# Kernel optimization log

Hardware: AMD Instinct MI355X
Metric: run time of the kernel (lower is better)

The kernel has to match this reference:

```python
import jax, jax.numpy as jnp
import numpy as np

K = 11      # kernel_size
PAD = 5     # (dilation*(K-1)+1 - 1)//2 with dilation=1


def _unfold(x, k, pad):
    # torch nn.Unfold ordering: channel slowest, then (ki, kj) fastest.
    B, C, H, W = x.shape
    xp = jnp.pad(x, ((0, 0), (0, 0), (pad, pad), (pad, pad)))
    # [B, C, k*k, H, W] -- small fixed loop over the 121 kernel offsets
    cols = jnp.stack([xp[:, :, i:i + H, j:j + W]
                      for i in range(k) for j in range(k)], axis=2)
    return cols.reshape(B, C * k * k, H * W)  # [B, 363, L]


def setup_inputs() -> dict:
    key = jax.random.key(0)
    ks = jax.random.split(key, 4)
    x = jax.random.normal(ks[0], (1, 3, 400, 400), dtype=jnp.float32)
    W1 = jax.random.normal(ks[1], (363, 128), dtype=jnp.float32) * 0.05
    b1 = jnp.zeros((128,), dtype=jnp.float32)
    W2 = jax.random.normal(ks[2], (128, 64), dtype=jnp.float32) * 0.08
    b2 = jnp.zeros((64,), dtype=jnp.float32)
    W3 = jax.random.normal(ks[3], (64, 8), dtype=jnp.float32) * 0.1
    b3 = jnp.zeros((8,), dtype=jnp.float32)
    return {"x": x, "W1": W1, "b1": b1, "W2": W2, "b2": b2, "W3": W3, "b3": b3}


def reference(x, W1, b1, W2, b2, W3, b3):
    B, C, H, W = x.shape
    cols = _unfold(x, K, PAD)                 # [B, 363, H*W]
    h = cols.transpose(0, 2, 1)               # [B, L, 363]
    h = jax.nn.leaky_relu(h @ W1 + b1)        # [B, L, 128], slope 0.01 = torch default
    h = jax.nn.leaky_relu(h @ W2 + b2)        # [B, L, 64]
    h = h @ W3 + b3                           # [B, L, 8]
    # Fold(kernel=1) is a reshape; squeeze(0) + permute -> [H, W, E]
    y = h[0].reshape(H, W, -1)
    # F.normalize(p=2, dim=-1, eps=1e-12)
    n = jnp.maximum(jnp.linalg.norm(y, axis=-1, keepdims=True), 1e-12)
    return y / n
```

## Files before the change

### kernel.cpp

```cpp
#include <hip/hip_runtime.h>
#include <hip/hip_bf16.h>
#include <math.h>

typedef _Float16 f16x8 __attribute__((ext_vector_type(8)));
typedef _Float16 f16x4 __attribute__((ext_vector_type(4)));
typedef float    f32x4 __attribute__((ext_vector_type(4)));

#define IMG   400
#define NPIX  160000
#define NKT1  18
#define W1P   (NKT1*8*64*8)
#define W2P   (4*4*64*8)
#define W3P   (2*64*8)
#define H1S   136
#define H2S   72
#define XPH   1938

__device__ __forceinline__ void async_cp16(const _Float16* g, _Float16* l) {
    __builtin_amdgcn_global_load_lds(
        (const __attribute__((address_space(1))) uint32_t*)g,
        (__attribute__((address_space(3))) uint32_t*)l, 16, 0, 0);
}

__global__ void pack_weights(const float* __restrict__ W1,
                             const float* __restrict__ W2,
                             const float* __restrict__ W3,
                             _Float16* __restrict__ ws)
{
    int i = blockIdx.x * blockDim.x + threadIdx.x;
    if (i < 576 * 128) {
        int kp = i >> 7, n = i & 127;
        int kt = kp >> 5, kl = kp & 31, q = kl >> 3, j = kl & 7;
        int pair = kp >> 4, kj = kp & 15;
        int c = pair / 12, ki = pair % 12;
        int mt = n >> 4, n15 = n & 15;
        int lane = q * 16 + n15;
        float v = (ki < 11 && kj < 11) ? W1[(c * 121 + ki * 11 + kj) * 128 + n] : 0.0f;
        ws[((kt * 8 + mt) * 64 + lane) * 8 + j] = (_Float16)v;
    } else if (i < 576 * 128 + 128 * 64) {
        int e = i - 576 * 128;
        int kp = e >> 6, n = e & 63;
        int kt = kp >> 5, kl = kp & 31, q = kl >> 3, j = kl & 7;
        int mt = n >> 4, n15 = n & 15;
        int lane = q * 16 + n15;
        ws[W1P + ((kt * 4 + mt) * 64 + lane) * 8 + j] = (_Float16)W2[kp * 64 + n];
    } else if (i < 576 * 128 + 128 * 64 + 64 * 16) {
        int e = i - 576 * 128 - 128 * 64;
        int kp = e >> 4, n = e & 15;
        int kt = kp >> 5, kl = kp & 31, q = kl >> 3, j = kl & 7;
        int lane = q * 16 + n;
        float v = (n < 8) ? W3[kp * 8 + n] : 0.0f;
        ws[W1P + W2P + (kt * 64 + lane) * 8 + j] = (_Float16)v;
    }
}

__global__ __launch_bounds__(256, 2) void fused_unfold_mlp(
    const float* __restrict__ x,
    const float* __restrict__ b1,
    const float* __restrict__ b2,
    const float* __restrict__ b3,
    const _Float16* __restrict__ wpack,
    float* __restrict__ out)
{
    __shared__ __align__(16) _Float16 xs[2 * XPH];
    __shared__ __align__(16) _Float16 hb[4 * 32 * H1S];
    __shared__ __align__(16) _Float16 w1s[2 * 4096];

    const int tid  = threadIdx.x;
    const int wave = tid >> 6;
    const int lane = tid & 63;
    const int q    = lane >> 4;
    const int n15  = lane & 15;
    const int bx   = blockIdx.x;
    const int by   = blockIdx.y;

    const _Float16* w1p = wpack;
    const _Float16* w2p = wpack + W1P;
    const _Float16* w3p = wpack + W1P + W2P;

    const int kt0 = (bx + by * 25) % NKT1;

    {
        int seg = wave * 2;
        async_cp16(w1p + kt0 * 4096 + seg * 512 + lane * 8, &w1s[seg * 512]);
        async_cp16(w1p + kt0 * 4096 + (seg + 1) * 512 + lane * 8, &w1s[(seg + 1) * 512]);
    }

    for (int w = tid; w < 3 * 19 * 35; w += 256) {
        int col = w % 35;
        int rc  = w / 35;
        int row = rc % 19, c = rc / 19;
        int gy = by * 8 + row - 5;
        int gx = bx * 16 + col - 6;
        float v = 0.0f;
        if ((unsigned)gy < (unsigned)IMG && (unsigned)gx < (unsigned)IMG)
            v = x[c * NPIX + gy * IMG + gx];
        _Float16 hv = (_Float16)v;
        int base = (c * 19 + row) * 34;
        if (col >= 1)  xs[base + col - 1] = hv;
        if (col <= 33) xs[XPH + base + col] = hv;
    }
    __syncthreads();

    _Float16* hw = &hb[wave * 32 * H1S];

    const uint32_t* xsd = (const uint32_t*)xs;
    const int h = q >> 1;
    const int u = n15 + (n15 & 1) + ((q & 1) << 3);
    const int bdw0 = (n15 & 1) * (XPH / 2) + (u >> 1);
    int bdwt[2];
#pragma unroll
    for (int t = 0; t < 2; ++t)
        bdwt[t] = bdw0 + (wave * 2 + t + h) * 17;

    f32x4 acc1[2][8];
#pragma unroll
    for (int t = 0; t < 2; ++t)
#pragma unroll
        for (int mt = 0; mt < 8; ++mt)
            acc1[t][mt] = (f32x4){0.f, 0.f, 0.f, 0.f};

    int kt = kt0;
    for (int kk = 0; kk < NKT1; ++kk) {
        if (kk) __syncthreads();
        const int buf  = kk & 1;
        const int nbuf = buf ^ 1;
        const int ktn  = (kt + 1 == NKT1) ? 0 : kt + 1;
        if (kk < NKT1 - 1) {
            int seg = wave * 2;
            async_cp16(w1p + ktn * 4096 + seg * 512 + lane * 8,
                       &w1s[nbuf * 4096 + seg * 512]);
            async_cp16(w1p + ktn * 4096 + (seg + 1) * 512 + lane * 8,
                       &w1s[nbuf * 4096 + (seg + 1) * 512]);
        }

        const int d6  = (kt >= 12) ? 2 : (kt >= 6 ? 1 : 0);
        const int m6  = kt - d6 * 6;
        const int rim = (d6 * 19 + 2 * m6) * 17;

        f16x8 bf[2];
#pragma unroll
        for (int t = 0; t < 2; ++t) {
            union { uint32_t u[4]; f16x8 f; } cv;
#pragma unroll
            for (int m = 0; m < 4; ++m)
                cv.u[m] = xsd[bdwt[t] + rim + m];
            bf[t] = cv.f;
        }
        const _Float16* wb = &w1s[buf * 4096];
#pragma unroll
        for (int mt = 0; mt < 8; ++mt) {
            f16x8 af = *(const f16x8*)(wb + (mt * 64 + lane) * 8);
            acc1[0][mt] = __builtin_amdgcn_mfma_f32_16x16x32_f16(af, bf[0], acc1[0][mt], 0, 0, 0);
            acc1[1][mt] = __builtin_amdgcn_mfma_f32_16x16x32_f16(af, bf[1], acc1[1][mt], 0, 0, 0);
        }
        kt = ktn;
    }

    f16x8 af2[4][4];
#pragma unroll
    for (int k2 = 0; k2 < 4; ++k2)
#pragma unroll
        for (int mt = 0; mt < 4; ++mt)
            af2[k2][mt] = *(const f16x8*)(w2p + ((k2 * 4 + mt) * 64 + lane) * 8);
    f16x8 af3[2];
#pragma unroll
    for (int k3 = 0; k3 < 2; ++k3)
        af3[k3] = *(const f16x8*)(w3p + (k3 * 64 + lane) * 8);

#pragma unroll
    for (int mt = 0; mt < 8; ++mt) {
        float4 bb = *(const float4*)(b1 + mt * 16 + q * 4);
#pragma unroll
        for (int t = 0; t < 2; ++t) {
            f16x4 hv;
#pragma unroll
            for (int r = 0; r < 4; ++r) {
                float v = acc1[t][mt][r] + ((const float*)&bb)[r];
                v = fmaxf(v, 0.01f * v);
                hv[r] = (_Float16)v;
            }
            *(f16x4*)(hw + (t * 16 + n15) * H1S + mt * 16 + q * 4) = hv;
        }
    }

    f32x4 acc2[2][4];
#pragma unroll
    for (int t = 0; t < 2; ++t)
#pragma unroll
        for (int mt = 0; mt < 4; ++mt)
            acc2[t][mt] = (f32x4){0.f, 0.f, 0.f, 0.f};

#pragma unroll
    for (int k2 = 0; k2 < 4; ++k2) {
        f16x8 bf[2];
#pragma unroll
        for (int t = 0; t < 2; ++t)
            bf[t] = *(const f16x8*)(hw + (t * 16 + n15) * H1S + k2 * 32 + q * 8);
#pragma unroll
        for (int mt = 0; mt < 4; ++mt) {
            acc2[0][mt] = __builtin_amdgcn_mfma_f32_16x16x32_f16(af2[k2][mt], bf[0], acc2[0][mt], 0, 0, 0);
            acc2[1][mt] = __builtin_amdgcn_mfma_f32_16x16x32_f16(af2[k2][mt], bf[1], acc2[1][mt], 0, 0, 0);
        }
    }

#pragma unroll
    for (int mt = 0; mt < 4; ++mt) {
        float4 bb = *(const float4*)(b2 + mt * 16 + q * 4);
#pragma unroll
        for (int t = 0; t < 2; ++t) {
            f16x4 hv;
#pragma unroll
            for (int r = 0; r < 4; ++r) {
                float v = acc2[t][mt][r] + ((const float*)&bb)[r];
                v = fmaxf(v, 0.01f * v);
                hv[r] = (_Float16)v;
            }
            *(f16x4*)(hw + (t * 16 + n15) * H2S + mt * 16 + q * 4) = hv;
        }
    }

    f32x4 acc3[2];
    acc3[0] = (f32x4){0.f, 0.f, 0.f, 0.f};
    acc3[1] = (f32x4){0.f, 0.f, 0.f, 0.f};
#pragma unroll
    for (int k3 = 0; k3 < 2; ++k3) {
#pragma unroll
        for (int t = 0; t < 2; ++t) {
            f16x8 bf = *(const f16x8*)(hw + (t * 16 + n15) * H2S + k3 * 32 + q * 8);
            acc3[t] = __builtin_amdgcn_mfma_f32_16x16x32_f16(af3[k3], bf, acc3[t], 0, 0, 0);
        }
    }

    float4 bb3 = make_float4(0.f, 0.f, 0.f, 0.f);
    if (q < 2) bb3 = *(const float4*)(b3 + q * 4);
#pragma unroll
    for (int t = 0; t < 2; ++t) {
        float v0 = acc3[t][0] + bb3.x;
        float v1 = acc3[t][1] + bb3.y;
        float v2 = acc3[t][2] + bb3.z;
        float v3 = acc3[t][3] + bb3.w;
        float s = v0 * v0 + v1 * v1 + v2 * v2 + v3 * v3;
        s += __shfl_xor(s, 16);
        s += __shfl_xor(s, 32);
        float inv = 1.0f / fmaxf(sqrtf(s), 1e-12f);
        if (q < 2) {
            int p = (by * 8 + wave * 2 + t) * IMG + bx * 16 + n15;
            float4 o = make_float4(v0 * inv, v1 * inv, v2 * inv, v3 * inv);
            *(float4*)(out + p * 8 + q * 4) = o;
        }
    }
}

extern "C" void kernel_launch(void* const* d_in, const int* in_sizes, int n_in,
                              void* d_out, int out_size, void* d_ws, size_t ws_size,
                              hipStream_t stream) {
    const float* x  = (const float*)d_in[0];
    const float* W1 = (const float*)d_in[1];
    const float* b1 = (const float*)d_in[2];
    const float* W2 = (const float*)d_in[3];
    const float* b2 = (const float*)d_in[4];
    const float* W3 = (const float*)d_in[5];
    const float* b3 = (const float*)d_in[6];
    float* out = (float*)d_out;
    _Float16* ws = (_Float16*)d_ws;

    pack_weights<<<dim3(324), dim3(256), 0, stream>>>(W1, W2, W3, ws);
    fused_unfold_mlp<<<dim3(25, 50), dim3(256), 0, stream>>>(x, b1, b2, b3, ws, out);
}
```

Measured before the change: 107.5 us.

## Shrink hidden-activation LDS staging and stream W2 through LDS to raise occupancy

Instead of writing the whole 128-wide layer-1 activation to LDS, each wave now writes and consumes 32-column chunks in a small 40-stride buffer, interleaved with the layer-2 MFMAs. W2 is copied into the freed W1 double buffer with async global-to-LDS loads rather than held in 16 register vectors. Launch bounds go from 2 to 4 blocks per CU. The aim is lower LDS and register use so more waves fit and hide latency. The cost is extra barriers and a serialized W2 copy, and the tighter register budget may cause spills.

```diff
diff --git a/kernel.cpp b/kernel.cpp
--- a/kernel.cpp
+++ b/kernel.cpp
@@ -12,8 +12,7 @@
 #define W1P   (NKT1*8*64*8)
 #define W2P   (4*4*64*8)
 #define W3P   (2*64*8)
-#define H1S   136
-#define H2S   72
+#define HSS   40
 #define XPH   1938
 
 __device__ __forceinline__ void async_cp16(const _Float16* g, _Float16* l) {
@@ -54,7 +53,7 @@
     }
 }
 
-__global__ __launch_bounds__(256, 2) void fused_unfold_mlp(
+__global__ __launch_bounds__(256, 4) void fused_unfold_mlp(
     const float* __restrict__ x,
     const float* __restrict__ b1,
     const float* __restrict__ b2,
@@ -63,8 +62,8 @@
     float* __restrict__ out)
 {
     __shared__ __align__(16) _Float16 xs[2 * XPH];
-    __shared__ __align__(16) _Float16 hb[4 * 32 * H1S];
     __shared__ __align__(16) _Float16 w1s[2 * 4096];
+    __shared__ __align__(16) _Float16 hs[4][32 * HSS];
 
     const int tid  = threadIdx.x;
     const int wave = tid >> 6;
@@ -102,8 +101,6 @@
     }
     __syncthreads();
 
-    _Float16* hw = &hb[wave * 32 * H1S];
-
     const uint32_t* xsd = (const uint32_t*)xs;
     const int h = q >> 1;
     const int u = n15 + (n15 & 1) + ((q & 1) << 3);
@@ -132,6 +129,12 @@
                        &w1s[nbuf * 4096 + seg * 512]);
             async_cp16(w1p + ktn * 4096 + (seg + 1) * 512 + lane * 8,
                        &w1s[nbuf * 4096 + (seg + 1) * 512]);
+        } else {
+            int seg = wave * 2;
+#pragma unroll
+            for (int s2 = 0; s2 < 2; ++s2)
+                async_cp16(w2p + (seg + s2) * 512 + lane * 8,
+                           &w1s[(seg + s2) * 512]);
         }
 
         const int d6  = (kt >= 12) ? 2 : (kt >= 6 ? 1 : 0);
@@ -156,69 +159,61 @@
         }
         kt = ktn;
     }
-
-    f16x8 af2[4][4];
-#pragma unroll
-    for (int k2 = 0; k2 < 4; ++k2)
+    __syncthreads();
+
+    {
+        int seg = wave * 2;
+#pragma unroll
+        for (int s2 = 0; s2 < 2; ++s2)
+            async_cp16(w2p + 4096 + (seg + s2) * 512 + lane * 8,
+                       &w1s[4096 + (seg + s2) * 512]);
+    }
+    __syncthreads();
+
+    const _Float16* w2s = w1s;
+    _Float16* hw = hs[wave];
+
+    f32x4 acc2[2][4];
+#pragma unroll
+    for (int t = 0; t < 2; ++t)
 #pragma unroll
         for (int mt = 0; mt < 4; ++mt)
-            af2[k2][mt] = *(const f16x8*)(w2p + ((k2 * 4 + mt) * 64 + lane) * 8);
+            acc2[t][mt] = (f32x4){0.f, 0.f, 0.f, 0.f};
+
+#pragma unroll
+    for (int k2 = 0; k2 < 4; ++k2) {
+#pragma unroll
+        for (int lm = 0; lm < 2; ++lm) {
+            int mt = 2 * k2 + lm;
+            float4 bb = *(const float4*)(b1 + mt * 16 + q * 4);
+#pragma unroll
+            for (int t = 0; t < 2; ++t) {
+                f16x4 hv;
+#pragma unroll
+                for (int r = 0; r < 4; ++r) {
+                    float v = acc1[t][mt][r] + ((const float*)&bb)[r];
+                    v = fmaxf(v, 0.01f * v);
+                    hv[r] = (_Float16)v;
+                }
+                *(f16x4*)(hw + (t * 16 + n15) * HSS + lm * 16 + q * 4) = hv;
+            }
+        }
+        f16x8 bf[2];
+#pragma unroll
+        for (int t = 0; t < 2; ++t)
+            bf[t] = *(const f16x8*)(hw + (t * 16 + n15) * HSS + q * 8);
+#pragma unroll
+        for (int mt2 = 0; mt2 < 4; ++mt2) {
+            f16x8 af = *(const f16x8*)(w2s + ((k2 * 4 + mt2) * 64 + lane) * 8);
+            acc2[0][mt2] = __builtin_amdgcn_mfma_f32_16x16x32_f16(af, bf[0], acc2[0][mt2], 0, 0, 0);
+            acc2[1][mt2] = __builtin_amdgcn_mfma_f32_16x16x32_f16(af, bf[1], acc2[1][mt2], 0, 0, 0);
+        }
+    }
+
     f16x8 af3[2];
 #pragma unroll
     for (int k3 = 0; k3 < 2; ++k3)
         af3[k3] = *(const f16x8*)(w3p + (k3 * 64 + lane) * 8);
-
-#pragma unroll
-    for (int mt = 0; mt < 8; ++mt) {
-        float4 bb = *(const float4*)(b1 + mt * 16 + q * 4);
-#pragma unroll
-        for (int t = 0; t < 2; ++t) {
-            f16x4 hv;
-#pragma unroll
-            for (int r = 0; r < 4; ++r) {
-                float v = acc1[t][mt][r] + ((const float*)&bb)[r];
-                v = fmaxf(v, 0.01f * v);
-                hv[r] = (_Float16)v;
-            }
-            *(f16x4*)(hw + (t * 16 + n15) * H1S + mt * 16 + q * 4) = hv;
-        }
-    }
-
-    f32x4 acc2[2][4];
-#pragma unroll
-    for (int t = 0; t < 2; ++t)
-#pragma unroll
-        for (int mt = 0; mt < 4; ++mt)
-            acc2[t][mt] = (f32x4){0.f, 0.f, 0.f, 0.f};
-
-#pragma unroll
-    for (int k2 = 0; k2 < 4; ++k2) {
-        f16x8 bf[2];
-#pragma unroll
-        for (int t = 0; t < 2; ++t)
-            bf[t] = *(const f16x8*)(hw + (t * 16 + n15) * H1S + k2 * 32 + q * 8);
-#pragma unroll
-        for (int mt = 0; mt < 4; ++mt) {
-            acc2[0][mt] = __builtin_amdgcn_mfma_f32_16x16x32_f16(af2[k2][mt], bf[0], acc2[0][mt], 0, 0, 0);
-            acc2[1][mt] = __builtin_amdgcn_mfma_f32_16x16x32_f16(af2[k2][mt], bf[1], acc2[1][mt], 0, 0, 0);
-        }
-    }
-
-#pragma unroll
-    for (int mt = 0; mt < 4; ++mt) {
-        float4 bb = *(const float4*)(b2 + mt * 16 + q * 4);
-#pragma unroll
-        for (int t = 0; t < 2; ++t) {
-            f16x4 hv;
-#pragma unroll
-            for (int r = 0; r < 4; ++r) {
-                float v = acc2[t][mt][r] + ((const float*)&bb)[r];
-                v = fmaxf(v, 0.01f * v);
-                hv[r] = (_Float16)v;
-            }
-            *(f16x4*)(hw + (t * 16 + n15) * H2S + mt * 16 + q * 4) = hv;
-        }
-    }
 
     f32x4 acc3[2];
     acc3[0] = (f32x4){0.f, 0.f, 0.f, 0.f};
@@ -226,8 +221,24 @@
 #pragma unroll
     for (int k3 = 0; k3 < 2; ++k3) {
 #pragma unroll
+        for (int lm = 0; lm < 2; ++lm) {
+            int mt2 = 2 * k3 + lm;
+            float4 bb = *(const float4*)(b2 + mt2 * 16 + q * 4);
+#pragma unroll
+            for (int t = 0; t < 2; ++t) {
+                f16x4 hv;
+#pragma unroll
+                for (int r = 0; r < 4; ++r) {
+                    float v = acc2[t][mt2][r] + ((const float*)&bb)[r];
+                    v = fmaxf(v, 0.01f * v);
+                    hv[r] = (_Float16)v;
+                }
+                *(f16x4*)(hw + (t * 16 + n15) * HSS + lm * 16 + q * 4) = hv;
+            }
+        }
+#pragma unroll
         for (int t = 0; t < 2; ++t) {
-            f16x8 bf = *(const f16x8*)(hw + (t * 16 + n15) * H2S + k3 * 32 + q * 8);
+            f16x8 bf = *(const f16x8*)(hw + (t * 16 + n15) * HSS + q * 8);
             acc3[t] = __builtin_amdgcn_mfma_f32_16x16x32_f16(af3[k3], bf, acc3[t], 0, 0, 0);
         }
     }
```

New measurement: 97.79 us. -9.1%, faster.
